# Kernel optimization log

Hardware: AMD Instinct MI355X
Metric: run time of the kernel (lower is better)

## Reference

```python
import jax, jax.numpy as jnp
import numpy as np

N_NODES = 100000
N_EDGES = 1600000
D = 64
N_GRAPHS = 64


def setup_inputs() -> dict:
    key = jax.random.key(0)
    ks = jax.random.split(key, 12)
    x = jax.random.normal(ks[0], (N_NODES, D), dtype=jnp.float32)
    edge_index = jax.random.randint(ks[1], (2, N_EDGES), 0, N_NODES, dtype=jnp.int32)
    batch = jnp.sort(jax.random.randint(ks[2], (N_NODES,), 0, N_GRAPHS, dtype=jnp.int32))
    s = 1.0 / np.sqrt(D)
    W1 = jax.random.uniform(ks[3], (D, D), jnp.float32, -s, s)
    b1 = jax.random.uniform(ks[4], (D,), jnp.float32, -s, s)
    W2 = jax.random.uniform(ks[5], (D, D), jnp.float32, -s, s)
    b2 = jax.random.uniform(ks[6], (D,), jnp.float32, -s, s)
    W3 = jax.random.uniform(ks[7], (D, D), jnp.float32, -s, s)
    b3 = jax.random.uniform(ks[8], (D,), jnp.float32, -s, s)
    lin_w = jax.random.uniform(ks[9], (D, 1), jnp.float32, -s, s)
    lin_b = jax.random.uniform(ks[10], (1,), jnp.float32, -s, s)
    return {"x": x, "edge_index": edge_index, "batch": batch,
            "W1": W1, "b1": b1, "W2": W2, "b2": b2, "W3": W3, "b3": b3,
            "lin_w": lin_w, "lin_b": lin_b}


def _gcn_conv(x, src, dst, norm, W, b):
    # PyG GCNConv: linear first, then normalized gather-scatter aggregation.
    h = x @ W                                   # [N, D]
    msg = h[src] * norm[:, None]                # [E+N, D] gathered + scaled
    out = jax.ops.segment_sum(msg, dst, num_segments=N_NODES)
    return out + b


def reference(x, edge_index, batch, W1, b1, W2, b2, W3, b3, lin_w, lin_b):
    loops = jnp.arange(N_NODES, dtype=edge_index.dtype)
    src = jnp.concatenate([edge_index[0], loops])  # source j
    dst = jnp.concatenate([edge_index[1], loops])  # target i
    # symmetric normalization D^{-1/2}(A+I)D^{-1/2}; deg >= 1 due to self loops
    deg = jax.ops.segment_sum(jnp.ones_like(dst, dtype=x.dtype), dst, num_segments=N_NODES)
    dis = jax.lax.rsqrt(deg)
    norm = dis[src] * dis[dst]                  # per-edge scalar
    h = jax.nn.relu(_gcn_conv(x, src, dst, norm, W1, b1))
    h = jax.nn.relu(_gcn_conv(h, src, dst, norm, W2, b2))
    h = jax.nn.relu(_gcn_conv(h, src, dst, norm, W3, b3))
    pooled = jax.ops.segment_sum(h, batch, num_segments=N_GRAPHS)  # global_add_pool
    return pooled @ lin_w + lin_b               # [N_GRAPHS, 1]
```

## Files before the change

kernel.cpp:

```cpp
#include <hip/hip_runtime.h>
#include <hip/hip_fp16.h>

#define D 64
#define NBMAX 512
#define BCAP 5120
#define TILE 64
#define ASTH 72
#define ACAP 448

typedef __attribute__((ext_vector_type(8))) short short8;
typedef __attribute__((ext_vector_type(4))) float float4v;

static __device__ __forceinline__ unsigned short f2bf(float x) {
    unsigned u = __float_as_uint(x);
    u += 0x7FFFu + ((u >> 16) & 1);
    return (unsigned short)(u >> 16);
}

__global__ void zero_ints(int* __restrict__ p, int n) {
    int i = blockIdx.x * blockDim.x + threadIdx.x;
    if (i < n) p[i] = 0;
}

__global__ void prescale_x(const float* __restrict__ x, const float* __restrict__ dis,
                           __half* __restrict__ out, int n2) {
    int i = blockIdx.x * blockDim.x + threadIdx.x;
    if (i < n2) {
        int n = i >> 5;
        float d = dis[n];
        float2 v = ((const float2*)x)[i];
        ((__half2*)out)[i] = __floats2half2_rn(v.x * d, v.y * d);
    }
}

__global__ __launch_bounds__(256) void bucket_scatter(const int* __restrict__ src,
                                                      const int* __restrict__ dst, int E,
                                                      int nb, int* __restrict__ gcursor,
                                                      unsigned* __restrict__ bpair) {
    __shared__ int lhist[NBMAX];
    __shared__ int lbase[NBMAX];
    int t = threadIdx.x;
    for (int i = t; i < nb; i += 256) lhist[i] = 0;
    __syncthreads();
    int e0 = blockIdx.x * 4096, e1 = min(e0 + 4096, E);
    for (int e = e0 + t; e < e1; e += 256) atomicAdd(&lhist[dst[e] >> 8], 1);
    __syncthreads();
    for (int i = t; i < nb; i += 256) {
        int c = lhist[i];
        lbase[i] = c ? atomicAdd(&gcursor[i], c) : 0;
        lhist[i] = 0;
    }
    __syncthreads();
    for (int e = e0 + t; e < e1; e += 256) {
        int d = dst[e];
        int b = d >> 8;
        int r = lbase[b] + atomicAdd(&lhist[b], 1);
        if (r < BCAP)
            bpair[(long)b * BCAP + r] = ((unsigned)src[e] << 8) | (unsigned)(d & 255);
    }
}

__global__ void scan_buckets(const int* __restrict__ gcursor, int B, int* __restrict__ gbase) {
    __shared__ int s[512];
    int t = threadIdx.x;
    s[t] = (t < B) ? gcursor[t] : 0;
    __syncthreads();
    for (int off = 1; off < 512; off <<= 1) {
        int v = (t >= off) ? s[t - off] : 0;
        __syncthreads();
        s[t] += v;
        __syncthreads();
    }
    if (t < B) gbase[t] = (t == 0) ? 0 : s[t - 1];
    if (t == 0) gbase[B] = s[511];
}

__global__ __launch_bounds__(256) void bucket_build(const unsigned* __restrict__ bpair,
                                                    int nb, int N,
                                                    const int* __restrict__ gcursor,
                                                    const int* __restrict__ gbase,
                                                    int* __restrict__ row_ptr,
                                                    float* __restrict__ dis,
                                                    int* __restrict__ adj) {
    __shared__ int hist[256];
    __shared__ int cur[256];
    __shared__ int wsum[4];
    int b = blockIdx.x, t = threadIdx.x;
    int cnt = gcursor[b];
    if (cnt > BCAP) cnt = BCAP;
    int ebase = gbase[b];
    const unsigned* bp = bpair + (long)b * BCAP;

    hist[t] = 0;
    __syncthreads();
    for (int i = t; i < cnt; i += 256) atomicAdd(&hist[bp[i] & 255u], 1);
    __syncthreads();
    int val = hist[t];
    int lane = t & 63, wv = t >> 6;
    int v = val;
#pragma unroll
    for (int off = 1; off < 64; off <<= 1) {
        int u = __shfl_up(v, off, 64);
        if (lane >= off) v += u;
    }
    if (lane == 63) wsum[wv] = v;
    __syncthreads();
    int wo = 0;
#pragma unroll
    for (int w = 0; w < 4; w++)
        if (w < wv) wo += wsum[w];
    int excl = wo + v - val;
    int node = (b << 8) + t;
    if (node < N) {
        row_ptr[node] = ebase + excl;
        dis[node] = rsqrtf((float)(val + 1));
    }
    cur[t] = ebase + excl;
    __syncthreads();
    for (int i = t; i < cnt; i += 256) {
        unsigned p = bp[i];
        unsigned dl = p & 255u;
        int pos = atomicAdd(&cur[dl], 1);
        adj[pos] = (int)((p >> 8) << 6) | (int)(dl & 63u);
    }
    if (b == 0 && t == 0) row_ptr[N] = gbase[nb];
}

template <int NB>
static __device__ __forceinline__ void tile_layer_body(const __half* __restrict__ in,
                                                       const int* __restrict__ row_ptr,
                                                       const int* __restrict__ adj,
                                                       const float* __restrict__ dis,
                                                       const float* __restrict__ Wg,
                                                       const float* __restrict__ bias,
                                                       __half* __restrict__ out,
                                                       int N, int scale_out) {
    __shared__ __align__(16) unsigned short accb[TILE * ASTH];
    __shared__ int adjbuf[4][ACAP];

    int t = threadIdx.x;
    int lane = t & 63;
    int w = t >> 6;
    int row = lane >> 2;
    int c = lane & 3;
    int col = lane & 15, quad = lane >> 4;

    int t0 = blockIdx.x * TILE;
    int wbase = t0 + w * 16;
    int node = wbase + row;

    int e0r = 0, e1r = 0;
    if (node < N) { e0r = row_ptr[node]; e1r = row_ptr[node + 1]; }

    const char* inb = (const char*)in;
    int* adjw = adjbuf[w];
    unsigned c16 = (unsigned)c * 16u;

    float a[16];
#pragma unroll
    for (int j = 0; j < 16; j++) a[j] = 0.f;

#define ADD16(xa, ya)                                                   \
    {                                                                   \
        const __half2* h0 = (const __half2*)&(xa);                      \
        const __half2* h1 = (const __half2*)&(ya);                      \
        _Pragma("unroll")                                               \
        for (int j = 0; j < 4; j++) {                                   \
            float2 f = __half22float2(h0[j]);                           \
            a[2 * j] += f.x; a[2 * j + 1] += f.y;                       \
        }                                                               \
        _Pragma("unroll")                                               \
        for (int j = 0; j < 4; j++) {                                   \
            float2 f = __half22float2(h1[j]);                           \
            a[8 + 2 * j] += f.x; a[8 + 2 * j + 1] += f.y;               \
        }                                                               \
    }

    if (node < N) {
        unsigned rb = (unsigned)node * 128u + c16;
        int4 xa = *(const int4*)(inb + rb);
        int4 xb = *(const int4*)(inb + rb + 64);
        ADD16(xa, xb)
    }

    int wn0 = min(wbase, N);
    int wn1 = min(wbase + 16, N);
    int eb_w = row_ptr[wn0];
    int ee_w = row_ptr[wn1];

    for (int base = eb_w; base < ee_w; base += ACAP) {
        int clen = min(ACAP, ee_w - base);
        for (int i = lane; i < clen; i += 64) adjw[i] = adj[base + i];
        __builtin_amdgcn_s_waitcnt(0);

        int ls = max(e0r - base, 0);
        int le = min(e1r - base, clen);
        int cnt = max(le - ls, 0);
        int kmax = cnt;
#pragma unroll
        for (int off = 32; off >= 1; off >>= 1) {
            int o = __shfl_xor(kmax, off, 64);
            kmax = max(kmax, o);
        }
        int sidx = min(ls, clen - 1);

        for (int k = 0; k < kmax; k += NB) {
            bool ok[NB];
            unsigned ro[NB];
            int4 xa[NB], xb[NB];
#pragma unroll
            for (int u = 0; u < NB; u++) {
                int idx = ls + k + u;
                ok[u] = idx < le;
                int pk = adjw[ok[u] ? idx : sidx];
                ro[u] = (unsigned)(pk >> 6) * 128u + c16;
            }
#pragma unroll
            for (int u = 0; u < NB; u++) {
                xa[u] = *(const int4*)(inb + ro[u]);
                xb[u] = *(const int4*)(inb + ro[u] + 64);
            }
#pragma unroll
            for (int u = 0; u < NB; u++)
                if (ok[u]) ADD16(xa[u], xb[u])
        }
    }
#undef ADD16

    float dA = (node < N) ? dis[node] : 0.f;
    unsigned short* ab = &accb[(w * 16 + row) * ASTH];
    unsigned pk[8];
#pragma unroll
    for (int j = 0; j < 8; j++)
        pk[j] = (unsigned)f2bf(a[2 * j] * dA) | ((unsigned)f2bf(a[2 * j + 1] * dA) << 16);
    *(int4*)(ab + 8 * c) = make_int4((int)pk[0], (int)pk[1], (int)pk[2], (int)pk[3]);
    *(int4*)(ab + 32 + 8 * c) = make_int4((int)pk[4], (int)pk[5], (int)pk[6], (int)pk[7]);
    __builtin_amdgcn_s_waitcnt(0);

    const unsigned short* arp = &accb[(w * 16 + col) * ASTH + quad * 8];
    short8 Af0 = *(const short8*)arp;
    short8 Af1 = *(const short8*)(arp + 32);

    float dnv[4];
#pragma unroll
    for (int r = 0; r < 4; r++) {
        int onode = t0 + w * 16 + quad * 4 + r;
        dnv[r] = (onode < N) ? (scale_out ? dis[onode] : 1.f) : 0.f;
    }

#pragma unroll
    for (int cc = 0; cc < 4; cc++) {
        short8 B0, B1;
#pragma unroll
        for (int j = 0; j < 8; j++) {
            B0[j] = (short)f2bf(Wg[(quad * 8 + j) * D + 16 * cc + col]);
            B1[j] = (short)f2bf(Wg[(32 + quad * 8 + j) * D + 16 * cc + col]);
        }
        float4v z = {0.f, 0.f, 0.f, 0.f};
        float4v v = __builtin_amdgcn_mfma_f32_16x16x32_bf16(Af0, B0, z, 0, 0, 0);
        v = __builtin_amdgcn_mfma_f32_16x16x32_bf16(Af1, B1, v, 0, 0, 0);
        float bc = bias[16 * cc + col];
#pragma unroll
        for (int r = 0; r < 4; r++) {
            int onode = t0 + w * 16 + quad * 4 + r;
            if (onode < N) {
                float vv = fmaxf(v[r] + bc, 0.f) * dnv[r];
                out[(long)onode * D + 16 * cc + col] = __float2half(vv);
            }
        }
    }
}

__global__ __launch_bounds__(256) void tile_layer(const __half* __restrict__ in,
                                                  const int* __restrict__ row_ptr,
                                                  const int* __restrict__ adj,
                                                  const float* __restrict__ dis,
                                                  const float* __restrict__ Wg,
                                                  const float* __restrict__ bias,
                                                  __half* __restrict__ out,
                                                  int N, int scale_out) {
    tile_layer_body<4>(in, row_ptr, adj, dis, Wg, bias, out, N, scale_out);
}

__global__ __launch_bounds__(256) void pool_partial(const __half* __restrict__ h,
                                                    const int* __restrict__ batch, int N,
                                                    int chunk, float* __restrict__ pooled) {
    int lane = threadIdx.x & 63;
    int wv = threadIdx.x >> 6;
    int c0 = blockIdx.x * chunk;
    int c1 = min(c0 + chunk, N);
    int g_cur = -1;
    float acc = 0.f;
    for (int n = c0 + wv; n < c1; n += 4) {
        int g = batch[n];
        if (g != g_cur) {
            if (g_cur >= 0) atomicAdd(&pooled[g_cur * D + lane], acc);
            g_cur = g;
            acc = 0.f;
        }
        acc += __half2float(h[n * D + lane]);
    }
    if (g_cur >= 0) atomicAdd(&pooled[g_cur * D + lane], acc);
}

__global__ void pool_linear(const float* __restrict__ pooled,
                            const float* __restrict__ lin_w,
                            const float* __restrict__ lin_b,
                            float* __restrict__ out, int G) {
    int lane = threadIdx.x & 63;
    int g = blockIdx.x * (blockDim.x >> 6) + (threadIdx.x >> 6);
    if (g >= G) return;
    float t = pooled[g * D + lane] * lin_w[lane];
#pragma unroll
    for (int off = 32; off >= 1; off >>= 1) t += __shfl_down(t, off, 64);
    if (lane == 0) out[g] = t + lin_b[0];
}

extern "C" void kernel_launch(void* const* d_in, const int* in_sizes, int n_in,
                              void* d_out, int out_size, void* d_ws, size_t ws_size,
                              hipStream_t stream) {
    const float* x      = (const float*)d_in[0];
    const int*   edges  = (const int*)d_in[1];
    const int*   batch  = (const int*)d_in[2];
    const float* W1     = (const float*)d_in[3];
    const float* b1     = (const float*)d_in[4];
    const float* W2     = (const float*)d_in[5];
    const float* b2     = (const float*)d_in[6];
    const float* W3     = (const float*)d_in[7];
    const float* b3     = (const float*)d_in[8];
    const float* lin_w  = (const float*)d_in[9];
    const float* lin_b  = (const float*)d_in[10];
    float* out = (float*)d_out;

    const int N = in_sizes[2];
    const int E = in_sizes[1] / 2;
    const int G = out_size;
    const int nb = (N + 255) >> 8;

    const int* e_src = edges;
    const int* e_dst = edges + E;

    auto al = [](long v) { return (v + 63) & ~63L; };
    long o_gcur   = 0;
    long o_pooled = al(o_gcur + NBMAX);
    long o_gbase  = al(o_pooled + (long)G * D);
    long o_rowptr = al(o_gbase + nb + 1);
    long o_dis    = al(o_rowptr + N + 1);
    long o_adjs   = al(o_dis + N);
    long o_xh     = al(o_adjs + E);
    long o_hA     = al(o_xh + (long)N * D / 2);
    long o_hB     = o_hA + (long)N * D;

    int*    gcursor = (int*)d_ws + o_gcur;
    float*  pooled  = (float*)d_ws + o_pooled;
    int*    gbase   = (int*)d_ws + o_gbase;
    int*    row_ptr = (int*)d_ws + o_rowptr;
    float*  dis     = (float*)d_ws + o_dis;
    int*    adj     = (int*)d_ws + o_adjs;
    __half* xh      = (__half*)((float*)d_ws + o_xh);
    __half* hA      = (__half*)((float*)d_ws + o_hA);
    __half* hB      = (__half*)((float*)d_ws + o_hB);
    unsigned* bpair = (unsigned*)hA;

    int nz = (int)(o_pooled + (long)G * D);
    zero_ints<<<(nz + 255) / 256, 256, 0, stream>>>((int*)d_ws, nz);

    bucket_scatter<<<(E + 4095) / 4096, 256, 0, stream>>>(e_src, e_dst, E, nb, gcursor, bpair);
    scan_buckets<<<1, 512, 0, stream>>>(gcursor, nb, gbase);
    bucket_build<<<nb, 256, 0, stream>>>(bpair, nb, N, gcursor, gbase, row_ptr, dis, adj);

    int n2 = N * D / 2;
    prescale_x<<<(n2 + 255) / 256, 256, 0, stream>>>(x, dis, xh, n2);

    const int tl_blocks = (N + TILE - 1) / TILE;
    tile_layer<<<tl_blocks, 256, 0, stream>>>(xh, row_ptr, adj, dis, W1, b1, hB, N, 1);
    tile_layer<<<tl_blocks, 256, 0, stream>>>(hB, row_ptr, adj, dis, W2, b2, hA, N, 1);
    tile_layer<<<tl_blocks, 256, 0, stream>>>(hA, row_ptr, adj, dis, W3, b3, hB, N, 0);

    const int pool_blocks = 512;
    const int chunk = (N + pool_blocks - 1) / pool_blocks;
    pool_partial<<<pool_blocks, 256, 0, stream>>>(hB, batch, N, chunk, pooled);
    pool_linear<<<(G + 3) / 4, 256, 0, stream>>>(pooled, lin_w, lin_b, out, G);
}
```

Baseline: 278.8 us.

## Stage bucket scatter through shared memory for contiguous global writes

The bucket scatter kernel now does a local counting sort of each 4096-edge chunk into LDS: a prefix scan over per-bucket counts, a scatter into a shared staging buffer, then a linear pass that binary-searches each slot's bucket and writes it to global memory. Consecutive threads therefore write consecutive addresses within each bucket run instead of scattering randomly. In exchange it adds a 512-entry scan, a binary search per edge and about 24KB of extra shared memory, which may lower occupancy.

```diff
diff --git a/kernel.cpp b/kernel.cpp
--- a/kernel.cpp
+++ b/kernel.cpp
@@ -38,25 +38,60 @@
                                                       int nb, int* __restrict__ gcursor,
                                                       unsigned* __restrict__ bpair) {
     __shared__ int lhist[NBMAX];
-    __shared__ int lbase[NBMAX];
+    __shared__ int gb[NBMAX];
+    __shared__ int s[NBMAX];
+    __shared__ int lofs[NBMAX + 1];
+    __shared__ int cur2[NBMAX];
+    __shared__ unsigned sbuf[4096];
+
     int t = threadIdx.x;
     for (int i = t; i < nb; i += 256) lhist[i] = 0;
     __syncthreads();
+
     int e0 = blockIdx.x * 4096, e1 = min(e0 + 4096, E);
+    int tot = e1 - e0;
     for (int e = e0 + t; e < e1; e += 256) atomicAdd(&lhist[dst[e] >> 8], 1);
     __syncthreads();
+
+    s[t] = (t < nb) ? lhist[t] : 0;
+    s[t + 256] = (t + 256 < nb) ? lhist[t + 256] : 0;
     for (int i = t; i < nb; i += 256) {
         int c = lhist[i];
-        lbase[i] = c ? atomicAdd(&gcursor[i], c) : 0;
-        lhist[i] = 0;
-    }
-    __syncthreads();
+        gb[i] = c ? atomicAdd(&gcursor[i], c) : 0;
+    }
+    __syncthreads();
+
+    for (int off = 1; off < 512; off <<= 1) {
+        int v0 = (t >= off) ? s[t - off] : 0;
+        int v1 = ((t + 256) >= off) ? s[t + 256 - off] : 0;
+        __syncthreads();
+        s[t] += v0;
+        s[t + 256] += v1;
+        __syncthreads();
+    }
+    lofs[t] = (t == 0) ? 0 : s[t - 1];
+    lofs[t + 256] = s[t + 255];
+    if (t == 0) lofs[nb] = tot;
+    __syncthreads();
+    for (int i = t; i < nb; i += 256) cur2[i] = lofs[i];
+    __syncthreads();
+
     for (int e = e0 + t; e < e1; e += 256) {
         int d = dst[e];
         int b = d >> 8;
-        int r = lbase[b] + atomicAdd(&lhist[b], 1);
-        if (r < BCAP)
-            bpair[(long)b * BCAP + r] = ((unsigned)src[e] << 8) | (unsigned)(d & 255);
+        int p = atomicAdd(&cur2[b], 1);
+        sbuf[p] = ((unsigned)src[e] << 8) | (unsigned)(d & 255);
+    }
+    __syncthreads();
+
+    for (int i = t; i < tot; i += 256) {
+        int lo = 0, hi = nb - 1;
+        while (lo < hi) {
+            int mid = (lo + hi + 1) >> 1;
+            if (lofs[mid] <= i) lo = mid; else hi = mid - 1;
+        }
+        int r = gb[lo] + (i - lofs[lo]);
+        if (r < BCAP) bpair[(long)lo * BCAP + r] = sbuf[i];
     }
 }
 
```

Result: slower. 287.8 us (+3.2%).

## Replace bucketed CSR build with global-atomic histogram, scan, and scatter

Applied to the files above, without the earlier changes.

Replaces the two-level bucket sort CSR construction (LDS-local histograms into fixed-capacity per-bucket staging arrays, then per-bucket build) with a direct counting sort: per-node global atomic histogram, a hierarchical scan, and a global-atomic scatter into adjacency. This removes the BCAP truncation risk and the intermediate pair buffer pass. In exchange it issues millions of global atomics on random node addresses and adds two extra kernel launches. Neighbor order within a row becomes nondeterministic.

```diff
diff --git a/kernel.cpp b/kernel.cpp
--- a/kernel.cpp
+++ b/kernel.cpp
@@ -3,7 +3,6 @@
 
 #define D 64
 #define NBMAX 512
-#define BCAP 5120
 #define TILE 64
 #define ASTH 72
 #define ACAP 448
@@ -33,37 +32,45 @@
     }
 }
 
-__global__ __launch_bounds__(256) void bucket_scatter(const int* __restrict__ src,
-                                                      const int* __restrict__ dst, int E,
-                                                      int nb, int* __restrict__ gcursor,
-                                                      unsigned* __restrict__ bpair) {
-    __shared__ int lhist[NBMAX];
-    __shared__ int lbase[NBMAX];
-    int t = threadIdx.x;
-    for (int i = t; i < nb; i += 256) lhist[i] = 0;
+__global__ __launch_bounds__(256) void edge_hist(const int* __restrict__ dst, int E,
+                                                 int* __restrict__ nodecnt) {
+    int i = blockIdx.x * blockDim.x + threadIdx.x;
+    int stride = gridDim.x * blockDim.x;
+    for (int e = i; e < E; e += stride) atomicAdd(&nodecnt[dst[e]], 1);
+}
+
+__global__ __launch_bounds__(256) void node_scanA(const int* __restrict__ nodecnt, int N,
+                                                  int* __restrict__ row_ptr,
+                                                  float* __restrict__ dis,
+                                                  int* __restrict__ btot) {
+    __shared__ int wsum[4];
+    int b = blockIdx.x, t = threadIdx.x;
+    int n = (b << 8) + t;
+    int val = (n < N) ? nodecnt[n] : 0;
+    int lane = t & 63, wv = t >> 6;
+    int v = val;
+#pragma unroll
+    for (int off = 1; off < 64; off <<= 1) {
+        int u = __shfl_up(v, off, 64);
+        if (lane >= off) v += u;
+    }
+    if (lane == 63) wsum[wv] = v;
     __syncthreads();
-    int e0 = blockIdx.x * 4096, e1 = min(e0 + 4096, E);
-    for (int e = e0 + t; e < e1; e += 256) atomicAdd(&lhist[dst[e] >> 8], 1);
-    __syncthreads();
-    for (int i = t; i < nb; i += 256) {
-        int c = lhist[i];
-        lbase[i] = c ? atomicAdd(&gcursor[i], c) : 0;
-        lhist[i] = 0;
-    }
-    __syncthreads();
-    for (int e = e0 + t; e < e1; e += 256) {
-        int d = dst[e];
-        int b = d >> 8;
-        int r = lbase[b] + atomicAdd(&lhist[b], 1);
-        if (r < BCAP)
-            bpair[(long)b * BCAP + r] = ((unsigned)src[e] << 8) | (unsigned)(d & 255);
-    }
-}
-
-__global__ void scan_buckets(const int* __restrict__ gcursor, int B, int* __restrict__ gbase) {
+    int wo = 0;
+#pragma unroll
+    for (int w = 0; w < 4; w++)
+        if (w < wv) wo += wsum[w];
+    if (n < N) {
+        row_ptr[n] = wo + v - val;
+        dis[n] = rsqrtf((float)(val + 1));
+    }
+    if (t == 255) btot[b] = wo + v;
+}
+
+__global__ void scan_buckets(const int* __restrict__ btot, int B, int* __restrict__ boff) {
     __shared__ int s[512];
     int t = threadIdx.x;
-    s[t] = (t < B) ? gcursor[t] : 0;
+    s[t] = (t < B) ? btot[t] : 0;
     __syncthreads();
     for (int off = 1; off < 512; off <<= 1) {
         int v = (t >= off) ? s[t - off] : 0;
@@ -71,59 +78,34 @@
         s[t] += v;
         __syncthreads();
     }
-    if (t < B) gbase[t] = (t == 0) ? 0 : s[t - 1];
-    if (t == 0) gbase[B] = s[511];
-}
-
-__global__ __launch_bounds__(256) void bucket_build(const unsigned* __restrict__ bpair,
-                                                    int nb, int N,
-                                                    const int* __restrict__ gcursor,
-                                                    const int* __restrict__ gbase,
-                                                    int* __restrict__ row_ptr,
-                                                    float* __restrict__ dis,
+    if (t < B) boff[t] = (t == 0) ? 0 : s[t - 1];
+    if (t == 0) boff[B] = s[511];
+}
+
+__global__ __launch_bounds__(256) void node_scanC(int* __restrict__ row_ptr,
+                                                  int* __restrict__ cursor,
+                                                  const int* __restrict__ boff,
+                                                  int N, int nbb) {
+    int n = blockIdx.x * blockDim.x + threadIdx.x;
+    if (n < N) {
+        int r = row_ptr[n] + boff[n >> 8];
+        row_ptr[n] = r;
+        cursor[n] = r;
+    }
+    if (n == 0) row_ptr[N] = boff[nbb];
+}
+
+__global__ __launch_bounds__(256) void edge_scatter(const int* __restrict__ src,
+                                                    const int* __restrict__ dst, int E,
+                                                    int* __restrict__ cursor,
                                                     int* __restrict__ adj) {
-    __shared__ int hist[256];
-    __shared__ int cur[256];
-    __shared__ int wsum[4];
-    int b = blockIdx.x, t = threadIdx.x;
-    int cnt = gcursor[b];
-    if (cnt > BCAP) cnt = BCAP;
-    int ebase = gbase[b];
-    const unsigned* bp = bpair + (long)b * BCAP;
-
-    hist[t] = 0;
-    __syncthreads();
-    for (int i = t; i < cnt; i += 256) atomicAdd(&hist[bp[i] & 255u], 1);
-    __syncthreads();
-    int val = hist[t];
-    int lane = t & 63, wv = t >> 6;
-    int v = val;
-#pragma unroll
-    for (int off = 1; off < 64; off <<= 1) {
-        int u = __shfl_up(v, off, 64);
-        if (lane >= off) v += u;
-    }
-    if (lane == 63) wsum[wv] = v;
-    __syncthreads();
-    int wo = 0;
-#pragma unroll
-    for (int w = 0; w < 4; w++)
-        if (w < wv) wo += wsum[w];
-    int excl = wo + v - val;
-    int node = (b << 8) + t;
-    if (node < N) {
-        row_ptr[node] = ebase + excl;
-        dis[node] = rsqrtf((float)(val + 1));
-    }
-    cur[t] = ebase + excl;
-    __syncthreads();
-    for (int i = t; i < cnt; i += 256) {
-        unsigned p = bp[i];
-        unsigned dl = p & 255u;
-        int pos = atomicAdd(&cur[dl], 1);
-        adj[pos] = (int)((p >> 8) << 6) | (int)(dl & 63u);
-    }
-    if (b == 0 && t == 0) row_ptr[N] = gbase[nb];
+    int i = blockIdx.x * blockDim.x + threadIdx.x;
+    int stride = gridDim.x * blockDim.x;
+    for (int e = i; e < E; e += stride) {
+        int d = dst[e];
+        int pos = atomicAdd(&cursor[d], 1);
+        adj[pos] = (src[e] << 6) | (d & 63);
+    }
 }
 
 template <int NB>
@@ -335,39 +317,44 @@
     const int N = in_sizes[2];
     const int E = in_sizes[1] / 2;
     const int G = out_size;
-    const int nb = (N + 255) >> 8;
+    const int nbb = (N + 255) >> 8;
 
     const int* e_src = edges;
     const int* e_dst = edges + E;
 
     auto al = [](long v) { return (v + 63) & ~63L; };
-    long o_gcur   = 0;
-    long o_pooled = al(o_gcur + NBMAX);
-    long o_gbase  = al(o_pooled + (long)G * D);
-    long o_rowptr = al(o_gbase + nb + 1);
-    long o_dis    = al(o_rowptr + N + 1);
-    long o_adjs   = al(o_dis + N);
-    long o_xh     = al(o_adjs + E);
-    long o_hA     = al(o_xh + (long)N * D / 2);
-    long o_hB     = o_hA + (long)N * D;
-
-    int*    gcursor = (int*)d_ws + o_gcur;
+    long o_nodecnt = 0;
+    long o_pooled  = al(o_nodecnt + N);
+    long o_btot    = al(o_pooled + (long)G * D);
+    long o_boff    = al(o_btot + NBMAX);
+    long o_rowptr  = al(o_boff + NBMAX + 1);
+    long o_cursor  = al(o_rowptr + N + 1);
+    long o_dis     = al(o_cursor + N);
+    long o_adjs    = al(o_dis + N);
+    long o_xh      = al(o_adjs + E);
+    long o_hA      = al(o_xh + (long)N * D / 2);
+    long o_hB      = al(o_hA + (long)N * D / 2);
+
+    int*    nodecnt = (int*)d_ws + o_nodecnt;
     float*  pooled  = (float*)d_ws + o_pooled;
-    int*    gbase   = (int*)d_ws + o_gbase;
+    int*    btot    = (int*)d_ws + o_btot;
+    int*    boff    = (int*)d_ws + o_boff;
     int*    row_ptr = (int*)d_ws + o_rowptr;
+    int*    cursor  = (int*)d_ws + o_cursor;
     float*  dis     = (float*)d_ws + o_dis;
     int*    adj     = (int*)d_ws + o_adjs;
     __half* xh      = (__half*)((float*)d_ws + o_xh);
     __half* hA      = (__half*)((float*)d_ws + o_hA);
     __half* hB      = (__half*)((float*)d_ws + o_hB);
-    unsigned* bpair = (unsigned*)hA;
 
     int nz = (int)(o_pooled + (long)G * D);
     zero_ints<<<(nz + 255) / 256, 256, 0, stream>>>((int*)d_ws, nz);
 
-    bucket_scatter<<<(E + 4095) / 4096, 256, 0, stream>>>(e_src, e_dst, E, nb, gcursor, bpair);
-    scan_buckets<<<1, 512, 0, stream>>>(gcursor, nb, gbase);
-    bucket_build<<<nb, 256, 0, stream>>>(bpair, nb, N, gcursor, gbase, row_ptr, dis, adj);
+    edge_hist<<<2048, 256, 0, stream>>>(e_dst, E, nodecnt);
+    node_scanA<<<nbb, 256, 0, stream>>>(nodecnt, N, row_ptr, dis, btot);
+    scan_buckets<<<1, 512, 0, stream>>>(btot, nbb, boff);
+    node_scanC<<<(N + 255) / 256, 256, 0, stream>>>(row_ptr, cursor, boff, N, nbb);
+    edge_scatter<<<2048, 256, 0, stream>>>(e_src, e_dst, E, cursor, adj);
 
     int n2 = N * D / 2;
     prescale_x<<<(n2 + 255) / 256, 256, 0, stream>>>(x, dis, xh, n2);
```

Result: slower. 441.0 us (+58.2%).
